# Kernel optimization log

Measured on AMD Instinct MI355X. Metric: run time of the kernel, lower is better.

The kernel has to match this reference:

```python
import jax, jax.numpy as jnp
import numpy as np

B, N_FEAT, SEQ, E, H, V = 32, 196, 64, 1024, 1024, 32000


def setup_inputs() -> dict:
    key = jax.random.key(0)
    ks = jax.random.split(key, 16)
    s = 0.02
    return {
        "features": jax.random.normal(ks[0], (B, N_FEAT, E), jnp.float32),
        "captions": jax.random.randint(ks[1], (B, SEQ), 0, V),
        "max_seq_length": SEQ,
        # decoder embedding table (vocab, embed)
        "emb": jax.random.normal(ks[2], (V, E), jnp.float32) * s,
        # attention MLP: Linear(E->H), Tanh, Linear(H->1)
        "Wa1": jax.random.normal(ks[3], (H, E), jnp.float32) * s,
        "ba1": jnp.zeros((H,), jnp.float32),
        "Wa2": jax.random.normal(ks[4], (1, H), jnp.float32) * s,
        "ba2": jnp.zeros((1,), jnp.float32),
        # GRU (1 layer), input = concat(word_emb, context) -> E + H
        "W_ih": jax.random.normal(ks[5], (3 * H, E + H), jnp.float32) * s,
        "W_hh": jax.random.normal(ks[6], (3 * H, H), jnp.float32) * s,
        "b_ih": jnp.zeros((3 * H,), jnp.float32),
        "b_hh": jnp.zeros((3 * H,), jnp.float32),
        # output projection Linear(H -> V)
        "W_fc": jax.random.normal(ks[7], (V, H), jnp.float32) * s,
        "b_fc": jnp.zeros((V,), jnp.float32),
    }


def reference(features, captions, max_seq_length, emb, Wa1, ba1, Wa2, ba2,
              W_ih, W_hh, b_ih, b_hh, W_fc, b_fc):
    # words: (B, S, E)
    words = emb[captions]
    # combined: (B, N_FEAT + S, E)
    combined = jnp.concatenate([features, words], axis=1)
    # attention scores over the combined tokens, softmax along token axis
    scores = jnp.tanh(combined @ Wa1.T + ba1) @ Wa2.T + ba2   # (B, M, 1)
    A = jax.nn.softmax(scores, axis=1)                         # (B, M, 1)
    # context h0 = A^T @ combined -> (B, E); used both as GRU h0 and per-step context
    h0 = jnp.sum(A * combined, axis=1)
    context = h0

    def gru_cell(x, h):
        gi = x @ W_ih.T + b_ih          # (B, 3H)
        gh = h @ W_hh.T + b_hh          # (B, 3H)
        ir, iz, inn = jnp.split(gi, 3, axis=-1)
        hr, hz, hn = jnp.split(gh, 3, axis=-1)
        r = jax.nn.sigmoid(ir + hr)
        z = jax.nn.sigmoid(iz + hz)
        n = jnp.tanh(inn + r * hn)
        return (1.0 - z) * n + z * h

    def step(carry, _):
        input_word, h = carry
        x = jnp.concatenate([emb[input_word], context], axis=-1)  # (B, E+H)
        h_new = gru_cell(x, h)
        out = h_new @ W_fc.T + b_fc                               # (B, V)
        # greedy feedback (eval path / no teacher forcing)
        next_word = jnp.argmax(out, axis=-1)
        return (next_word, h_new), out

    init = (captions[:, 0], h0)
    (_, _), outs = jax.lax.scan(step, init, None, length=max_seq_length - 1)
    outs = jnp.transpose(outs, (1, 0, 2))                         # (B, S-1, V)
    bsz = captions.shape[0]
    vocab = W_fc.shape[0]
    outputs = jnp.concatenate(
        [jnp.zeros((bsz, 1, vocab), outs.dtype), outs], axis=1)   # t=0 stays zero
    return outputs, A
```

## Files before the change

kernel.cpp:

```cpp
#include <hip/hip_runtime.h>
#include <hip/hip_bf16.h>

typedef unsigned long long ull;
typedef unsigned int uint;

#define NB 32
#define NFEAT 196
#define SEQL 64
#define ED 1024
#define HD 1024
#define VOC 32000
#define NCOMB 260
#define NROWS (NB*NCOMB)
#define NTILE 2000

typedef __attribute__((ext_vector_type(8))) short s16x8;
typedef __attribute__((ext_vector_type(4))) float f32x4;
typedef __attribute__((ext_vector_type(4))) uint  u32x4;

union FragU { u32x4 u; s16x8 s; };

#define DOT4(acc, wv, xv) acc = fmaf((wv).x,(xv).x, fmaf((wv).y,(xv).y, fmaf((wv).z,(xv).z, fmaf((wv).w,(xv).w,(acc)))))

__device__ __forceinline__ uint enc_f32(float f) {
    uint u = __float_as_uint(f);
    return (u & 0x80000000u) ? ~u : (u | 0x80000000u);
}
__device__ __forceinline__ ull shflxor64(ull v, int m) {
    uint lo = __shfl_xor((uint)v, m);
    uint hi = __shfl_xor((uint)(v >> 32), m);
    return (((ull)hi) << 32) | (ull)lo;
}

__device__ __forceinline__ void split2(float a, float b, uint& hi, uint& lo) {
    __hip_bfloat162 h2 = __float22bfloat162_rn(make_float2(a, b));
    float2 hf = __bfloat1622float2(h2);
    __hip_bfloat162 l2 = __float22bfloat162_rn(make_float2(a - hf.x, b - hf.y));
    hi = *(uint*)&h2;
    lo = *(uint*)&l2;
}

__global__ void __launch_bounds__(256) k_build(
    const float* __restrict__ features, const int* __restrict__ captions,
    const float* __restrict__ emb, float* __restrict__ combined,
    float* __restrict__ out)
{
    const int bid = blockIdx.x;
    const int t = threadIdx.x;
    if (bid < NROWS) {
        const int b = bid / NCOMB;
        const int i = bid - b*NCOMB;
        const float* src = (i < NFEAT)
            ? (features + ((size_t)(b*NFEAT + i))*ED)
            : (emb + (size_t)captions[b*SEQL + (i - NFEAT)]*ED);
        float4* dst4 = (float4*)(combined + (size_t)bid*ED);
        const float4* s4 = (const float4*)src;
        dst4[t] = s4[t];
    } else {
        const int z = bid - NROWS;
        const int m = z*1024 + t*4;
        if (m < NB*VOC) {
            const int b = m / VOC;
            const int v = m - b*VOC;
            float4 zz = make_float4(0.f,0.f,0.f,0.f);
            *(float4*)(out + (size_t)b*((size_t)SEQL*VOC) + v) = zz;
        }
    }
}

__global__ void __launch_bounds__(256) k_pack_w1(
    const float* __restrict__ Wa1, uint* __restrict__ W1hi, uint* __restrict__ W1lo)
{
    const int eid = blockIdx.x*256 + threadIdx.x;
    const int lane = eid & 63;
    const int ks = (eid >> 6) & 31;
    const int ct = eid >> 11;
    const int c = ct*16 + (lane & 15);
    const int k0 = ks*32 + ((lane >> 4) & 3)*4;
    const float4 wa = *(const float4*)&Wa1[(size_t)c*ED + k0];
    const float4 wb = *(const float4*)&Wa1[(size_t)c*ED + k0 + 16];
    uint hi[4], lo[4];
    split2(wa.x, wa.y, hi[0], lo[0]);
    split2(wa.z, wa.w, hi[1], lo[1]);
    split2(wb.x, wb.y, hi[2], lo[2]);
    split2(wb.z, wb.w, hi[3], lo[3]);
    *(u32x4*)&W1hi[(size_t)eid*4] = (u32x4){hi[0], hi[1], hi[2], hi[3]};
    *(u32x4*)&W1lo[(size_t)eid*4] = (u32x4){lo[0], lo[1], lo[2], lo[3]};
}

__global__ void __launch_bounds__(256) k_pack_wfc(
    const float* __restrict__ W_fc, uint* __restrict__ Whi, uint* __restrict__ Wlo)
{
    const int eid = blockIdx.x*256 + threadIdx.x;
    const int lane = eid & 63;
    const int ks = (eid >> 6) & 31;
    const int tile = eid >> 11;
    const int row = tile*16 + (lane & 15);
    const int k0 = ks*32 + ((lane >> 4) & 3)*4;
    const float4 wa = *(const float4*)&W_fc[(size_t)row*HD + k0];
    const float4 wb = *(const float4*)&W_fc[(size_t)row*HD + k0 + 16];
    uint hi[4], lo[4];
    split2(wa.x, wa.y, hi[0], lo[0]);
    split2(wa.z, wa.w, hi[1], lo[1]);
    split2(wb.x, wb.y, hi[2], lo[2]);
    split2(wb.z, wb.w, hi[3], lo[3]);
    *(u32x4*)&Whi[(size_t)eid*4] = (u32x4){hi[0], hi[1], hi[2], hi[3]};
    *(u32x4*)&Wlo[(size_t)eid*4] = (u32x4){lo[0], lo[1], lo[2], lo[3]};
}

__global__ void __launch_bounds__(256) k_attn_mfma(
    const float* __restrict__ combined, const uint* __restrict__ W1hi,
    const uint* __restrict__ W1lo, const float* __restrict__ ba1,
    const float* __restrict__ Wa2, float* __restrict__ partials)
{
    const int t = threadIdx.x;
    const int w = t >> 6, l = t & 63;
    const int lane16 = l & 15, qk = (l >> 4) & 3;
    const int rt = blockIdx.x*4 + w;
    const int cg = blockIdx.y;

    const float* Arow = combined + (size_t)(rt*16 + lane16)*ED;
    const u32x4* bh_base = (const u32x4*)W1hi + (size_t)(cg*4)*32*64 + l;
    const u32x4* bl_base = (const u32x4*)W1lo + (size_t)(cg*4)*32*64 + l;

    f32x4 acc[4];
#pragma unroll
    for (int i = 0; i < 4; ++i) acc[i] = (f32x4){0.f,0.f,0.f,0.f};

#pragma unroll 2
    for (int ks = 0; ks < 32; ++ks) {
        const int k0 = ks*32 + qk*4;
        const float4 aa = *(const float4*)(Arow + k0);
        const float4 ab = *(const float4*)(Arow + k0 + 16);
        FragU ahi, alo;
        uint h0,l0_,h1,l1_,h2,l2_,h3,l3_;
        split2(aa.x, aa.y, h0, l0_);
        split2(aa.z, aa.w, h1, l1_);
        split2(ab.x, ab.y, h2, l2_);
        split2(ab.z, ab.w, h3, l3_);
        ahi.u = (u32x4){h0, h1, h2, h3};
        alo.u = (u32x4){l0_, l1_, l2_, l3_};
#pragma unroll
        for (int i = 0; i < 4; ++i) {
            FragU bh_, bl_;
            bh_.u = bh_base[((size_t)i*32 + ks)*64];
            bl_.u = bl_base[((size_t)i*32 + ks)*64];
            acc[i] = __builtin_amdgcn_mfma_f32_16x16x32_bf16(ahi.s, bh_.s, acc[i], 0, 0, 0);
            acc[i] = __builtin_amdgcn_mfma_f32_16x16x32_bf16(ahi.s, bl_.s, acc[i], 0, 0, 0);
            acc[i] = __builtin_amdgcn_mfma_f32_16x16x32_bf16(alo.s, bh_.s, acc[i], 0, 0, 0);
        }
    }

    float s[4];
#pragma unroll
    for (int r = 0; r < 4; ++r) {
        float sum = 0.f;
#pragma unroll
        for (int i = 0; i < 4; ++i) {
            const int col = cg*64 + i*16 + lane16;
            sum += tanhf(acc[i][r] + ba1[col]) * Wa2[col];
        }
        s[r] = sum;
    }
#pragma unroll
    for (int m = 1; m <= 8; m <<= 1)
#pragma unroll
        for (int r = 0; r < 4; ++r) s[r] += __shfl_xor(s[r], m);
    if (lane16 == 0) {
#pragma unroll
        for (int r = 0; r < 4; ++r)
            partials[(size_t)(rt*16 + qk*4 + r)*16 + cg] = s[r];
    }
}

__global__ void __launch_bounds__(256) k_attn_finish(
    const float* __restrict__ partials, const float* __restrict__ combined,
    const int* __restrict__ captions,
    float* __restrict__ A_out, float* __restrict__ h0,
    float* __restrict__ ctx, ull* __restrict__ slots0)
{
    const int b = blockIdx.x, t = threadIdx.x;
    __shared__ float sc[NCOMB];
    __shared__ float red[256];

    for (int i = t; i < NCOMB; i += 256) {
        float s = 0.f;
        const float* pr = partials + (size_t)(b*NCOMB + i)*16;
#pragma unroll
        for (int g = 0; g < 16; ++g) s += pr[g];
        sc[i] = s;
    }
    __syncthreads();
    float m = -1e30f;
    for (int i = t; i < NCOMB; i += 256) m = fmaxf(m, sc[i]);
    red[t] = m; __syncthreads();
    for (int s2 = 128; s2 > 0; s2 >>= 1) {
        if (t < s2) red[t] = fmaxf(red[t], red[t+s2]);
        __syncthreads();
    }
    m = red[0]; __syncthreads();
    float ssum = 0.f;
    for (int i = t; i < NCOMB; i += 256) { float e = expf(sc[i] - m); sc[i] = e; ssum += e; }
    red[t] = ssum; __syncthreads();
    for (int s2 = 128; s2 > 0; s2 >>= 1) {
        if (t < s2) red[t] += red[t+s2];
        __syncthreads();
    }
    const float S = red[0]; __syncthreads();
    for (int i = t; i < NCOMB; i += 256) {
        const float a = sc[i] / S;
        sc[i] = a;
        A_out[b*NCOMB + i] = a;
    }
    __syncthreads();
    for (int e = t; e < HD; e += 256) {
        float acc = 0.f;
        const float* cb = combined + (size_t)b*NCOMB*ED + e;
        for (int i = 0; i < NCOMB; ++i) acc = fmaf(sc[i], cb[(size_t)i*ED], acc);
        h0[(size_t)b*HD + e] = acc;
        ctx[(size_t)b*HD + e] = acc;
    }
    if (t == 0) {
        slots0[0*NB + b] = (ull)(~(uint)captions[b*SEQL]);
#pragma unroll
        for (int g = 1; g < 8; ++g) slots0[g*NB + b] = 0ull;
    }
}

__global__ void __launch_bounds__(256) k_gru(
    const float* __restrict__ emb, const float* __restrict__ ctx,
    const float* __restrict__ W_ih, const float* __restrict__ W_hh,
    const float* __restrict__ b_ih, const float* __restrict__ b_hh,
    const float* __restrict__ h_prev, float* __restrict__ h_next,
    const ull* __restrict__ slots_prev, ull* __restrict__ slots_cur,
    uint* __restrict__ Hhi, uint* __restrict__ Hlo)
{
    __shared__ int word_s[NB];
    const int t = threadIdx.x;
    if (t < NB) {
        ull best = 0ull;
#pragma unroll
        for (int g = 0; g < 8; ++g) {
            ull k = slots_prev[g*NB + t];
            best = (k > best) ? k : best;
        }
        word_s[t] = (int)(~(uint)best);
    }
    if (blockIdx.x == 0) slots_cur[t] = 0ull;
    __syncthreads();

    const int j = blockIdx.x;
    const int w = t >> 6, l = t & 63;
    const int b0 = w*8;

    float a[4][8];
#pragma unroll
    for (int g = 0; g < 4; ++g)
#pragma unroll
        for (int i = 0; i < 8; ++i) a[g][i] = 0.f;

    const float* Wr = W_ih + (size_t)j*(ED+HD);
    const float* Wz = W_ih + (size_t)(HD + j)*(ED+HD);
    const float* Wn = W_ih + (size_t)(2*HD + j)*(ED+HD);
#pragma unroll
    for (int q = 0; q < 8; ++q) {
        const int k = q*256 + l*4;
        const float4 wr = *(const float4*)(Wr + k);
        const float4 wz = *(const float4*)(Wz + k);
        const float4 wn = *(const float4*)(Wn + k);
#pragma unroll
        for (int i = 0; i < 8; ++i) {
            const int b = b0 + i;
            const float* xs = (q < 4) ? (emb + (size_t)word_s[b]*ED + k)
                                      : (ctx + (size_t)b*HD + (k - ED));
            const float4 xv = *(const float4*)xs;
            DOT4(a[0][i], wr, xv);
            DOT4(a[1][i], wz, xv);
            DOT4(a[2][i], wn, xv);
        }
    }
    const float* Ur = W_hh + (size_t)j*HD;
    const float* Uz = W_hh + (size_t)(HD + j)*HD;
    const float* Un = W_hh + (size_t)(2*HD + j)*HD;
#pragma unroll
    for (int q = 0; q < 4; ++q) {
        const int k = q*256 + l*4;
        const float4 ur = *(const float4*)(Ur + k);
        const float4 uz = *(const float4*)(Uz + k);
        const float4 un = *(const float4*)(Un + k);
#pragma unroll
        for (int i = 0; i < 8; ++i) {
            const int b = b0 + i;
            const float4 hv = *(const float4*)(h_prev + (size_t)b*HD + k);
            DOT4(a[0][i], ur, hv);
            DOT4(a[1][i], uz, hv);
            DOT4(a[3][i], un, hv);
        }
    }
    int s = (l >> 5) & 1;
    int ib = s*4;
    float tA[4][4];
#pragma unroll
    for (int g = 0; g < 4; ++g)
#pragma unroll
        for (int ii = 0; ii < 4; ++ii) {
            const float send = a[g][(1^s)*4 + ii];
            tA[g][ii] = a[g][s*4 + ii] + __shfl_xor(send, 32);
        }
    s = (l >> 4) & 1; ib += s*2;
    float tB[4][2];
#pragma unroll
    for (int g = 0; g < 4; ++g)
#pragma unroll
        for (int jj = 0; jj < 2; ++jj) {
            const float send = tA[g][(1^s)*2 + jj];
            tB[g][jj] = tA[g][s*2 + jj] + __shfl_xor(send, 16);
        }
    s = (l >> 3) & 1; ib += s;
    float fg[4];
#pragma unroll
    for (int g = 0; g < 4; ++g) {
        const float send = tB[g][1^s];
        fg[g] = tB[g][s] + __shfl_xor(send, 8);
    }
#pragma unroll
    for (int mm = 4; mm >= 1; mm >>= 1)
#pragma unroll
        for (int g = 0; g < 4; ++g) fg[g] += __shfl_xor(fg[g], mm);

    if ((l & 7) == 0) {
        const int b = b0 + ib;
        const float rg = 1.f/(1.f + expf(-(fg[0] + b_ih[j]      + b_hh[j])));
        const float zg = 1.f/(1.f + expf(-(fg[1] + b_ih[HD+j]   + b_hh[HD+j])));
        const float ng = tanhf(fg[2] + b_ih[2*HD+j] + rg*(fg[3] + b_hh[2*HD+j]));
        const float hp = h_prev[(size_t)b*HD + j];
        const float hv = (1.f - zg)*ng + zg*hp;
        h_next[(size_t)b*HD + j] = hv;
        __hip_bfloat16 hb = __float2bfloat16(hv);
        const float hf = __bfloat162float(hb);
        __hip_bfloat16 lb = __float2bfloat16(hv - hf);
        const int bh = b >> 4;
        const int ks = j >> 5;
        const int qk2 = (j >> 2) & 3;
        const int elem = (j & 3) + 4*((j >> 4) & 1);
        const size_t ei = (((size_t)(bh*32 + ks))*64 + qk2*16 + (b & 15))*8 + elem;
        ((ushort*)Hhi)[ei] = *(const ushort*)&hb;
        ((ushort*)Hlo)[ei] = *(const ushort*)&lb;
    }
}

__global__ void __launch_bounds__(256) k_logits(
    const float* __restrict__ W_fc, const uint* __restrict__ Wfchi,
    const uint* __restrict__ Wfclo, const uint* __restrict__ Hhi,
    const uint* __restrict__ Hlo, const float* __restrict__ b_fc,
    float* __restrict__ out, ull* __restrict__ slots_cur, int tstep, int packed)
{
    __shared__ float sm[32][68];
    const int t = threadIdx.x;
    const int w = t >> 6, l = t & 63;
    const int lane16 = l & 15, qk = (l >> 4) & 3;
    const int tile = blockIdx.x*4 + w;
    const int row = tile*16 + lane16;

    const u32x4* hh0 = (const u32x4*)Hhi + l;
    const u32x4* hl0 = (const u32x4*)Hlo + l;
    const u32x4* hh1 = (const u32x4*)Hhi + 2048 + l;
    const u32x4* hl1 = (const u32x4*)Hlo + 2048 + l;

    f32x4 acc0 = {0.f,0.f,0.f,0.f};
    f32x4 acc1 = {0.f,0.f,0.f,0.f};

    if (packed) {
        const u32x4* WH = (const u32x4*)Wfchi + (size_t)tile*32*64 + l;
        const u32x4* WL = (const u32x4*)Wfclo + (size_t)tile*32*64 + l;
#pragma unroll 2
        for (int ks = 0; ks < 32; ++ks) {
            FragU whi, wlo, b0h, b0l, b1h, b1l;
            whi.u = WH[ks*64];
            wlo.u = WL[ks*64];
            b0h.u = hh0[ks*64];
            b0l.u = hl0[ks*64];
            b1h.u = hh1[ks*64];
            b1l.u = hl1[ks*64];
            acc0 = __builtin_amdgcn_mfma_f32_16x16x32_bf16(whi.s, b0h.s, acc0, 0, 0, 0);
            acc0 = __builtin_amdgcn_mfma_f32_16x16x32_bf16(whi.s, b0l.s, acc0, 0, 0, 0);
            acc0 = __builtin_amdgcn_mfma_f32_16x16x32_bf16(wlo.s, b0h.s, acc0, 0, 0, 0);
            acc1 = __builtin_amdgcn_mfma_f32_16x16x32_bf16(whi.s, b1h.s, acc1, 0, 0, 0);
            acc1 = __builtin_amdgcn_mfma_f32_16x16x32_bf16(whi.s, b1l.s, acc1, 0, 0, 0);
            acc1 = __builtin_amdgcn_mfma_f32_16x16x32_bf16(wlo.s, b1h.s, acc1, 0, 0, 0);
        }
    } else {
        const float* Wrow = W_fc + (size_t)row*HD;
#pragma unroll 2
        for (int ks = 0; ks < 32; ++ks) {
            const int k0 = ks*32 + qk*4;
            const float4 wa = *(const float4*)(Wrow + k0);
            const float4 wb = *(const float4*)(Wrow + k0 + 16);
            FragU whi, wlo;
            uint h0,l0_,h1,l1_,h2,l2_,h3,l3_;
            split2(wa.x, wa.y, h0, l0_);
            split2(wa.z, wa.w, h1, l1_);
            split2(wb.x, wb.y, h2, l2_);
            split2(wb.z, wb.w, h3, l3_);
            whi.u = (u32x4){h0, h1, h2, h3};
            wlo.u = (u32x4){l0_, l1_, l2_, l3_};
            FragU b0h, b0l, b1h, b1l;
            b0h.u = hh0[ks*64];
            b0l.u = hl0[ks*64];
            b1h.u = hh1[ks*64];
            b1l.u = hl1[ks*64];
            acc0 = __builtin_amdgcn_mfma_f32_16x16x32_bf16(whi.s, b0h.s, acc0, 0, 0, 0);
            acc0 = __builtin_amdgcn_mfma_f32_16x16x32_bf16(whi.s, b0l.s, acc0, 0, 0, 0);
            acc0 = __builtin_amdgcn_mfma_f32_16x16x32_bf16(wlo.s, b0h.s, acc0, 0, 0, 0);
            acc1 = __builtin_amdgcn_mfma_f32_16x16x32_bf16(whi.s, b1h.s, acc1, 0, 0, 0);
            acc1 = __builtin_amdgcn_mfma_f32_16x16x32_bf16(whi.s, b1l.s, acc1, 0, 0, 0);
            acc1 = __builtin_amdgcn_mfma_f32_16x16x32_bf16(wlo.s, b1h.s, acc1, 0, 0, 0);
        }
    }

    {
        const int rbase = w*16 + qk*4;
        const float4 bias = *(const float4*)&b_fc[blockIdx.x*64 + rbase];
        *(float4*)&sm[lane16][rbase] = make_float4(
            acc0[0] + bias.x, acc0[1] + bias.y, acc0[2] + bias.z, acc0[3] + bias.w);
        *(float4*)&sm[16 + lane16][rbase] = make_float4(
            acc1[0] + bias.x, acc1[1] + bias.y, acc1[2] + bias.z, acc1[3] + bias.w);
    }
    __syncthreads();
    {
        const int b = t >> 3;
        const int rl0 = (t & 7)*8;
        const int vbase = blockIdx.x*64 + rl0;
        float v[8];
        ull bk = 0ull;
#pragma unroll
        for (int e = 0; e < 8; ++e) {
            v[e] = sm[b][rl0 + e];
            const ull key = (((ull)enc_f32(v[e])) << 32) | (ull)(~(uint)(vbase + e));
            bk = (key > bk) ? key : bk;
        }
        float* dst = out + (size_t)b*((size_t)SEQL*VOC) + (size_t)tstep*VOC + vbase;
        ((float4*)dst)[0] = make_float4(v[0], v[1], v[2], v[3]);
        ((float4*)dst)[1] = make_float4(v[4], v[5], v[6], v[7]);
#pragma unroll
        for (int mm = 4; mm >= 1; mm >>= 1) {
            const ull o = shflxor64(bk, mm);
            bk = (o > bk) ? o : bk;
        }
        if ((t & 7) == 0) atomicMax(slots_cur + (blockIdx.x & 7)*NB + b, bk);
    }
}

extern "C" void kernel_launch(void* const* d_in, const int* in_sizes, int n_in,
                              void* d_out, int out_size, void* d_ws, size_t ws_size,
                              hipStream_t stream)
{
    const float* features = (const float*)d_in[0];
    const int*   captions = (const int*)d_in[1];
    const float* emb  = (const float*)d_in[3];
    const float* Wa1  = (const float*)d_in[4];
    const float* ba1  = (const float*)d_in[5];
    const float* Wa2  = (const float*)d_in[6];
    const float* W_ih = (const float*)d_in[8];
    const float* W_hh = (const float*)d_in[9];
    const float* b_ih = (const float*)d_in[10];
    const float* b_hh = (const float*)d_in[11];
    const float* W_fc = (const float*)d_in[12];
    const float* b_fc = (const float*)d_in[13];

    float* out = (float*)d_out;
    float* A_out = out + (size_t)NB*SEQL*VOC;

    char* wsp = (char*)d_ws;
    float* combined = (float*)wsp;  wsp += (size_t)NROWS*ED*4;
    float* partials = (float*)wsp;  wsp += (size_t)NROWS*16*4;
    float* hbuf0    = (float*)wsp;  wsp += (size_t)NB*HD*4;
    float* hbuf1    = (float*)wsp;  wsp += (size_t)NB*HD*4;
    float* ctx      = (float*)wsp;  wsp += (size_t)NB*HD*4;
    ull*   slots    = (ull*)wsp;    wsp += 2*8*NB*sizeof(ull);
    uint*  Hhi      = (uint*)wsp;   wsp += (size_t)4096*16;
    uint*  Hlo      = (uint*)wsp;   wsp += (size_t)4096*16;
    uint*  W1hi     = (uint*)wsp;   wsp += (size_t)131072*16;
    uint*  W1lo     = (uint*)wsp;   wsp += (size_t)131072*16;
    uint*  Wfchi    = (uint*)wsp;   wsp += (size_t)NTILE*32*64*16;
    uint*  Wfclo    = (uint*)wsp;   wsp += (size_t)NTILE*32*64*16;
    size_t packed_need = (size_t)(wsp - (char*)d_ws);
    const int packed = (ws_size >= packed_need) ? 1 : 0;

    k_build<<<NROWS + 1000, 256, 0, stream>>>(features, captions, emb, combined, out);
    k_pack_w1<<<512, 256, 0, stream>>>(Wa1, W1hi, W1lo);
    if (packed)
        k_pack_wfc<<<NTILE*32*64/256, 256, 0, stream>>>(W_fc, Wfchi, Wfclo);
    k_attn_mfma<<<dim3(130, 16), 256, 0, stream>>>(combined, W1hi, W1lo, ba1, Wa2, partials);
    k_attn_finish<<<NB, 256, 0, stream>>>(partials, combined, captions,
                                          A_out, hbuf0, ctx, slots);
    for (int t = 1; t < SEQL; ++t) {
        const float* hp = (t & 1) ? hbuf0 : hbuf1;
        float*       hn = (t & 1) ? hbuf1 : hbuf0;
        const ull* sp = slots + (size_t)((t - 1) & 1)*8*NB;
        ull*       scur = slots + (size_t)(t & 1)*8*NB;
        k_gru<<<1024, 256, 0, stream>>>(emb, ctx, W_ih, W_hh, b_ih, b_hh,
                                        hp, hn, sp, scur, Hhi, Hlo);
        k_logits<<<500, 256, 0, stream>>>(W_fc, Wfchi, Wfclo, Hhi, Hlo, b_fc,
                                          out, scur, t, packed);
    }
}
```

Before: 4.442 ms.

## Split logits K across waves and widen attention column groups per block

The logits kernel now gives each block two 16-row vocab tiles, each split over two K halves handled by separate waves. The halves are merged through shared memory before bias add and argmax, and the grid doubles to 1000 blocks. The aim is more parallelism and shorter per-wave dependent MFMA chains in the latency-bound per-step logits GEMM, at the cost of an extra barrier and an LDS reduction. Separately, the attention MFMA kernel has each block compute two column groups so the A-fragment split is reused, halving its grid.

```diff
diff --git a/kernel.cpp b/kernel.cpp
--- a/kernel.cpp
+++ b/kernel.cpp
@@ -117,15 +117,17 @@
     const int w = t >> 6, l = t & 63;
     const int lane16 = l & 15, qk = (l >> 4) & 3;
     const int rt = blockIdx.x*4 + w;
-    const int cg = blockIdx.y;
+    const int cg0 = blockIdx.y*2;
 
     const float* Arow = combined + (size_t)(rt*16 + lane16)*ED;
-    const u32x4* bh_base = (const u32x4*)W1hi + (size_t)(cg*4)*32*64 + l;
-    const u32x4* bl_base = (const u32x4*)W1lo + (size_t)(cg*4)*32*64 + l;
-
-    f32x4 acc[4];
-#pragma unroll
-    for (int i = 0; i < 4; ++i) acc[i] = (f32x4){0.f,0.f,0.f,0.f};
+    const u32x4* bh_base = (const u32x4*)W1hi + l;
+    const u32x4* bl_base = (const u32x4*)W1lo + l;
+
+    f32x4 acc[2][4];
+#pragma unroll
+    for (int c = 0; c < 2; ++c)
+#pragma unroll
+        for (int i = 0; i < 4; ++i) acc[c][i] = (f32x4){0.f,0.f,0.f,0.f};
 
 #pragma unroll 2
     for (int ks = 0; ks < 32; ++ks) {
@@ -141,35 +143,43 @@
         ahi.u = (u32x4){h0, h1, h2, h3};
         alo.u = (u32x4){l0_, l1_, l2_, l3_};
 #pragma unroll
-        for (int i = 0; i < 4; ++i) {
-            FragU bh_, bl_;
-            bh_.u = bh_base[((size_t)i*32 + ks)*64];
-            bl_.u = bl_base[((size_t)i*32 + ks)*64];
-            acc[i] = __builtin_amdgcn_mfma_f32_16x16x32_bf16(ahi.s, bh_.s, acc[i], 0, 0, 0);
-            acc[i] = __builtin_amdgcn_mfma_f32_16x16x32_bf16(ahi.s, bl_.s, acc[i], 0, 0, 0);
-            acc[i] = __builtin_amdgcn_mfma_f32_16x16x32_bf16(alo.s, bh_.s, acc[i], 0, 0, 0);
-        }
-    }
-
-    float s[4];
-#pragma unroll
-    for (int r = 0; r < 4; ++r) {
-        float sum = 0.f;
-#pragma unroll
-        for (int i = 0; i < 4; ++i) {
-            const int col = cg*64 + i*16 + lane16;
-            sum += tanhf(acc[i][r] + ba1[col]) * Wa2[col];
-        }
-        s[r] = sum;
-    }
-#pragma unroll
-    for (int m = 1; m <= 8; m <<= 1)
-#pragma unroll
-        for (int r = 0; r < 4; ++r) s[r] += __shfl_xor(s[r], m);
-    if (lane16 == 0) {
-#pragma unroll
-        for (int r = 0; r < 4; ++r)
-            partials[(size_t)(rt*16 + qk*4 + r)*16 + cg] = s[r];
+        for (int c = 0; c < 2; ++c) {
+#pragma unroll
+            for (int i = 0; i < 4; ++i) {
+                const size_t idx = (((size_t)((cg0 + c)*4 + i))*32 + ks)*64;
+                FragU bh_, bl_;
+                bh_.u = bh_base[idx];
+                bl_.u = bl_base[idx];
+                acc[c][i] = __builtin_amdgcn_mfma_f32_16x16x32_bf16(ahi.s, bh_.s, acc[c][i], 0, 0, 0);
+                acc[c][i] = __builtin_amdgcn_mfma_f32_16x16x32_bf16(ahi.s, bl_.s, acc[c][i], 0, 0, 0);
+                acc[c][i] = __builtin_amdgcn_mfma_f32_16x16x32_bf16(alo.s, bh_.s, acc[c][i], 0, 0, 0);
+            }
+        }
+    }
+
+#pragma unroll
+    for (int c = 0; c < 2; ++c) {
+        const int cg = cg0 + c;
+        float s[4];
+#pragma unroll
+        for (int r = 0; r < 4; ++r) {
+            float sum = 0.f;
+#pragma unroll
+            for (int i = 0; i < 4; ++i) {
+                const int col = cg*64 + i*16 + lane16;
+                sum += tanhf(acc[c][i][r] + ba1[col]) * Wa2[col];
+            }
+            s[r] = sum;
+        }
+#pragma unroll
+        for (int m = 1; m <= 8; m <<= 1)
+#pragma unroll
+            for (int r = 0; r < 4; ++r) s[r] += __shfl_xor(s[r], m);
+        if (lane16 == 0) {
+#pragma unroll
+            for (int r = 0; r < 4; ++r)
+                partials[(size_t)(rt*16 + qk*4 + r)*16 + cg] = s[r];
+        }
     }
 }
 
@@ -355,26 +365,29 @@
     const uint* __restrict__ Hlo, const float* __restrict__ b_fc,
     float* __restrict__ out, ull* __restrict__ slots_cur, int tstep, int packed)
 {
-    __shared__ float sm[32][68];
+    __shared__ float sm[32][33];
+    __shared__ float mergebuf[2][64][8];
     const int t = threadIdx.x;
     const int w = t >> 6, l = t & 63;
     const int lane16 = l & 15, qk = (l >> 4) & 3;
-    const int tile = blockIdx.x*4 + w;
+    const int tt = w & 1;
+    const int kh = w >> 1;
+    const int tile = blockIdx.x*2 + tt;
     const int row = tile*16 + lane16;
 
-    const u32x4* hh0 = (const u32x4*)Hhi + l;
-    const u32x4* hl0 = (const u32x4*)Hlo + l;
-    const u32x4* hh1 = (const u32x4*)Hhi + 2048 + l;
-    const u32x4* hl1 = (const u32x4*)Hlo + 2048 + l;
+    const u32x4* hh0 = (const u32x4*)Hhi + (size_t)(kh*16)*64 + l;
+    const u32x4* hl0 = (const u32x4*)Hlo + (size_t)(kh*16)*64 + l;
+    const u32x4* hh1 = (const u32x4*)Hhi + (size_t)(32 + kh*16)*64 + l;
+    const u32x4* hl1 = (const u32x4*)Hlo + (size_t)(32 + kh*16)*64 + l;
 
     f32x4 acc0 = {0.f,0.f,0.f,0.f};
     f32x4 acc1 = {0.f,0.f,0.f,0.f};
 
     if (packed) {
-        const u32x4* WH = (const u32x4*)Wfchi + (size_t)tile*32*64 + l;
-        const u32x4* WL = (const u32x4*)Wfclo + (size_t)tile*32*64 + l;
+        const u32x4* WH = (const u32x4*)Wfchi + ((size_t)tile*32 + kh*16)*64 + l;
+        const u32x4* WL = (const u32x4*)Wfclo + ((size_t)tile*32 + kh*16)*64 + l;
 #pragma unroll 2
-        for (int ks = 0; ks < 32; ++ks) {
+        for (int ks = 0; ks < 16; ++ks) {
             FragU whi, wlo, b0h, b0l, b1h, b1l;
             whi.u = WH[ks*64];
             wlo.u = WL[ks*64];
@@ -392,8 +405,8 @@
     } else {
         const float* Wrow = W_fc + (size_t)row*HD;
 #pragma unroll 2
-        for (int ks = 0; ks < 32; ++ks) {
-            const int k0 = ks*32 + qk*4;
+        for (int ks = 0; ks < 16; ++ks) {
+            const int k0 = (kh*16 + ks)*32 + qk*4;
             const float4 wa = *(const float4*)(Wrow + k0);
             const float4 wb = *(const float4*)(Wrow + k0 + 16);
             FragU whi, wlo;
@@ -418,36 +431,44 @@
         }
     }
 
-    {
-        const int rbase = w*16 + qk*4;
-        const float4 bias = *(const float4*)&b_fc[blockIdx.x*64 + rbase];
-        *(float4*)&sm[lane16][rbase] = make_float4(
-            acc0[0] + bias.x, acc0[1] + bias.y, acc0[2] + bias.z, acc0[3] + bias.w);
-        *(float4*)&sm[16 + lane16][rbase] = make_float4(
-            acc1[0] + bias.x, acc1[1] + bias.y, acc1[2] + bias.z, acc1[3] + bias.w);
+    if (kh == 1) {
+        float* rr = &mergebuf[tt][l][0];
+        *(float4*)&rr[0] = make_float4(acc0[0], acc0[1], acc0[2], acc0[3]);
+        *(float4*)&rr[4] = make_float4(acc1[0], acc1[1], acc1[2], acc1[3]);
+    }
+    __syncthreads();
+    if (kh == 0) {
+        const float* rr = &mergebuf[tt][l][0];
+        const float4 bias = *(const float4*)&b_fc[tile*16 + qk*4];
+#pragma unroll
+        for (int r = 0; r < 4; ++r) {
+            const int rloc = tt*16 + qk*4 + r;
+            const float bb = (&bias.x)[r];
+            sm[lane16][rloc]      = acc0[r] + rr[r]     + bb;
+            sm[16 + lane16][rloc] = acc1[r] + rr[4 + r] + bb;
+        }
     }
     __syncthreads();
     {
         const int b = t >> 3;
-        const int rl0 = (t & 7)*8;
-        const int vbase = blockIdx.x*64 + rl0;
-        float v[8];
+        const int rq = t & 7;
+        const int vbase = blockIdx.x*32 + rq*4;
+        float v[4];
         ull bk = 0ull;
 #pragma unroll
-        for (int e = 0; e < 8; ++e) {
-            v[e] = sm[b][rl0 + e];
+        for (int e = 0; e < 4; ++e) {
+            v[e] = sm[b][rq*4 + e];
             const ull key = (((ull)enc_f32(v[e])) << 32) | (ull)(~(uint)(vbase + e));
             bk = (key > bk) ? key : bk;
         }
-        float* dst = out + (size_t)b*((size_t)SEQL*VOC) + (size_t)tstep*VOC + vbase;
-        ((float4*)dst)[0] = make_float4(v[0], v[1], v[2], v[3]);
-        ((float4*)dst)[1] = make_float4(v[4], v[5], v[6], v[7]);
+        *(float4*)&out[(size_t)b*((size_t)SEQL*VOC) + (size_t)tstep*VOC + vbase] =
+            make_float4(v[0], v[1], v[2], v[3]);
 #pragma unroll
         for (int mm = 4; mm >= 1; mm >>= 1) {
             const ull o = shflxor64(bk, mm);
             bk = (o > bk) ? o : bk;
         }
-        if ((t & 7) == 0) atomicMax(slots_cur + (blockIdx.x & 7)*NB + b, bk);
+        if (rq == 0) atomicMax(slots_cur + (blockIdx.x & 7)*NB + b, bk);
     }
 }
 
@@ -491,7 +512,7 @@
     k_pack_w1<<<512, 256, 0, stream>>>(Wa1, W1hi, W1lo);
     if (packed)
         k_pack_wfc<<<NTILE*32*64/256, 256, 0, stream>>>(W_fc, Wfchi, Wfclo);
-    k_attn_mfma<<<dim3(130, 16), 256, 0, stream>>>(combined, W1hi, W1lo, ba1, Wa2, partials);
+    k_attn_mfma<<<dim3(130, 8), 256, 0, stream>>>(combined, W1hi, W1lo, ba1, Wa2, partials);
     k_attn_finish<<<NB, 256, 0, stream>>>(partials, combined, captions,
                                           A_out, hbuf0, ctx, slots);
     for (int t = 1; t < SEQL; ++t) {
@@ -501,7 +522,7 @@
         ull*       scur = slots + (size_t)(t & 1)*8*NB;
         k_gru<<<1024, 256, 0, stream>>>(emb, ctx, W_ih, W_hh, b_ih, b_hh,
                                         hp, hn, sp, scur, Hhi, Hlo);
-        k_logits<<<500, 256, 0, stream>>>(W_fc, Wfchi, Wfclo, Hhi, Hlo, b_fc,
-                                          out, scur, t, packed);
-    }
-}
+        k_logits<<<NTILE/2, 256, 0, stream>>>(W_fc, Wfchi, Wfclo, Hhi, Hlo, b_fc,
+                                              out, scur, t, packed);
+    }
+}
```

Result: slower. 4.565 ms (+2.8%).

## Fuse logits and next-step GRU via grid barrier; precompute context input gates

Applied to the files above, without the earlier changes.

Merges the per-step logits and the following GRU update into one kernel. Blocks write logits and argmax partials, then meet at an atomic-counter grid barrier, after which each block computes the GRU for a slice of hidden units for the next step. The constant context part of the input-gate product (W_ih times ctx plus b_ih) is now computed once up front in a new kernel instead of at every step. The attention MFMA kernel also handles two column groups per block. This halves the number of per-step launches and drops the redundant context GEMV, but the spin barrier assumes all 500 blocks are resident at the same time, and the GRU work is spread over only 500 blocks.

```diff
diff --git a/kernel.cpp b/kernel.cpp
--- a/kernel.cpp
+++ b/kernel.cpp
@@ -13,6 +13,7 @@
 #define NCOMB 260
 #define NROWS (NB*NCOMB)
 #define NTILE 2000
+#define STEPBLK 500
 
 typedef __attribute__((ext_vector_type(8))) short s16x8;
 typedef __attribute__((ext_vector_type(4))) float f32x4;
@@ -43,7 +44,7 @@
 __global__ void __launch_bounds__(256) k_build(
     const float* __restrict__ features, const int* __restrict__ captions,
     const float* __restrict__ emb, float* __restrict__ combined,
-    float* __restrict__ out)
+    float* __restrict__ out, uint* __restrict__ counters)
 {
     const int bid = blockIdx.x;
     const int t = threadIdx.x;
@@ -56,7 +57,7 @@
         float4* dst4 = (float4*)(combined + (size_t)bid*ED);
         const float4* s4 = (const float4*)src;
         dst4[t] = s4[t];
-    } else {
+    } else if (bid < NROWS + 1000) {
         const int z = bid - NROWS;
         const int m = z*1024 + t*4;
         if (m < NB*VOC) {
@@ -65,6 +66,8 @@
             float4 zz = make_float4(0.f,0.f,0.f,0.f);
             *(float4*)(out + (size_t)b*((size_t)SEQL*VOC) + v) = zz;
         }
+    } else {
+        if (t < SEQL) counters[t] = 0u;
     }
 }
 
@@ -117,15 +120,17 @@
     const int w = t >> 6, l = t & 63;
     const int lane16 = l & 15, qk = (l >> 4) & 3;
     const int rt = blockIdx.x*4 + w;
-    const int cg = blockIdx.y;
+    const int cg0 = blockIdx.y*2;
 
     const float* Arow = combined + (size_t)(rt*16 + lane16)*ED;
-    const u32x4* bh_base = (const u32x4*)W1hi + (size_t)(cg*4)*32*64 + l;
-    const u32x4* bl_base = (const u32x4*)W1lo + (size_t)(cg*4)*32*64 + l;
-
-    f32x4 acc[4];
-#pragma unroll
-    for (int i = 0; i < 4; ++i) acc[i] = (f32x4){0.f,0.f,0.f,0.f};
+    const u32x4* bh_base = (const u32x4*)W1hi + l;
+    const u32x4* bl_base = (const u32x4*)W1lo + l;
+
+    f32x4 acc[2][4];
+#pragma unroll
+    for (int c = 0; c < 2; ++c)
+#pragma unroll
+        for (int i = 0; i < 4; ++i) acc[c][i] = (f32x4){0.f,0.f,0.f,0.f};
 
 #pragma unroll 2
     for (int ks = 0; ks < 32; ++ks) {
@@ -141,35 +146,43 @@
         ahi.u = (u32x4){h0, h1, h2, h3};
         alo.u = (u32x4){l0_, l1_, l2_, l3_};
 #pragma unroll
-        for (int i = 0; i < 4; ++i) {
-            FragU bh_, bl_;
-            bh_.u = bh_base[((size_t)i*32 + ks)*64];
-            bl_.u = bl_base[((size_t)i*32 + ks)*64];
-            acc[i] = __builtin_amdgcn_mfma_f32_16x16x32_bf16(ahi.s, bh_.s, acc[i], 0, 0, 0);
-            acc[i] = __builtin_amdgcn_mfma_f32_16x16x32_bf16(ahi.s, bl_.s, acc[i], 0, 0, 0);
-            acc[i] = __builtin_amdgcn_mfma_f32_16x16x32_bf16(alo.s, bh_.s, acc[i], 0, 0, 0);
-        }
-    }
-
-    float s[4];
-#pragma unroll
-    for (int r = 0; r < 4; ++r) {
-        float sum = 0.f;
-#pragma unroll
-        for (int i = 0; i < 4; ++i) {
-            const int col = cg*64 + i*16 + lane16;
-            sum += tanhf(acc[i][r] + ba1[col]) * Wa2[col];
-        }
-        s[r] = sum;
-    }
-#pragma unroll
-    for (int m = 1; m <= 8; m <<= 1)
-#pragma unroll
-        for (int r = 0; r < 4; ++r) s[r] += __shfl_xor(s[r], m);
-    if (lane16 == 0) {
-#pragma unroll
-        for (int r = 0; r < 4; ++r)
-            partials[(size_t)(rt*16 + qk*4 + r)*16 + cg] = s[r];
+        for (int c = 0; c < 2; ++c) {
+#pragma unroll
+            for (int i = 0; i < 4; ++i) {
+                const size_t idx = (((size_t)((cg0 + c)*4 + i))*32 + ks)*64;
+                FragU bh_, bl_;
+                bh_.u = bh_base[idx];
+                bl_.u = bl_base[idx];
+                acc[c][i] = __builtin_amdgcn_mfma_f32_16x16x32_bf16(ahi.s, bh_.s, acc[c][i], 0, 0, 0);
+                acc[c][i] = __builtin_amdgcn_mfma_f32_16x16x32_bf16(ahi.s, bl_.s, acc[c][i], 0, 0, 0);
+                acc[c][i] = __builtin_amdgcn_mfma_f32_16x16x32_bf16(alo.s, bh_.s, acc[c][i], 0, 0, 0);
+            }
+        }
+    }
+
+#pragma unroll
+    for (int c = 0; c < 2; ++c) {
+        const int cg = cg0 + c;
+        float s[4];
+#pragma unroll
+        for (int r = 0; r < 4; ++r) {
+            float sum = 0.f;
+#pragma unroll
+            for (int i = 0; i < 4; ++i) {
+                const int col = cg*64 + i*16 + lane16;
+                sum += tanhf(acc[c][i][r] + ba1[col]) * Wa2[col];
+            }
+            s[r] = sum;
+        }
+#pragma unroll
+        for (int m = 1; m <= 8; m <<= 1)
+#pragma unroll
+            for (int r = 0; r < 4; ++r) s[r] += __shfl_xor(s[r], m);
+        if (lane16 == 0) {
+#pragma unroll
+            for (int r = 0; r < 4; ++r)
+                partials[(size_t)(rt*16 + qk*4 + r)*16 + cg] = s[r];
+        }
     }
 }
 
@@ -225,6 +238,56 @@
 #pragma unroll
         for (int g = 1; g < 8; ++g) slots0[g*NB + b] = 0ull;
     }
+}
+
+__global__ void __launch_bounds__(256) k_gictx(
+    const float* __restrict__ W_ih, const float* __restrict__ b_ih,
+    const float* __restrict__ ctx, float* __restrict__ gictx)
+{
+    const int jj = blockIdx.x;
+    const int t = threadIdx.x;
+    const int w = t >> 6, l = t & 63;
+    const int b0 = w*8;
+    const float* Wrow = W_ih + (size_t)jj*(ED+HD) + ED;
+
+    float a[8];
+#pragma unroll
+    for (int i = 0; i < 8; ++i) a[i] = 0.f;
+#pragma unroll
+    for (int q = 0; q < 4; ++q) {
+        const int k = q*256 + l*4;
+        const float4 wv = *(const float4*)(Wrow + k);
+#pragma unroll
+        for (int i = 0; i < 8; ++i) {
+            const float4 xv = *(const float4*)(ctx + (size_t)(b0 + i)*HD + k);
+            DOT4(a[i], wv, xv);
+        }
+    }
+    int s = (l >> 5) & 1;
+    int ib = s*4;
+    float tA[4];
+#pragma unroll
+    for (int ii = 0; ii < 4; ++ii) {
+        const float send = a[(1^s)*4 + ii];
+        tA[ii] = a[s*4 + ii] + __shfl_xor(send, 32);
+    }
+    s = (l >> 4) & 1; ib += s*2;
+    float tB[2];
+#pragma unroll
+    for (int jj2 = 0; jj2 < 2; ++jj2) {
+        const float send = tA[(1^s)*2 + jj2];
+        tB[jj2] = tA[s*2 + jj2] + __shfl_xor(send, 16);
+    }
+    s = (l >> 3) & 1; ib += s;
+    float fg;
+    {
+        const float send = tB[1^s];
+        fg = tB[s] + __shfl_xor(send, 8);
+    }
+#pragma unroll
+    for (int mm = 4; mm >= 1; mm >>= 1) fg += __shfl_xor(fg, mm);
+    if ((l & 7) == 0)
+        gictx[(size_t)jj*NB + (b0 + ib)] = fg + b_ih[jj];
 }
 
 __global__ void __launch_bounds__(256) k_gru(
@@ -349,106 +412,255 @@
     }
 }
 
-__global__ void __launch_bounds__(256) k_logits(
-    const float* __restrict__ W_fc, const uint* __restrict__ Wfchi,
-    const uint* __restrict__ Wfclo, const uint* __restrict__ Hhi,
-    const uint* __restrict__ Hlo, const float* __restrict__ b_fc,
-    float* __restrict__ out, ull* __restrict__ slots_cur, int tstep, int packed)
+__device__ __forceinline__ void gru_one_j(
+    int j, const int* word_s, const float* __restrict__ emb,
+    const float* __restrict__ W_ih, const float* __restrict__ W_hh,
+    const float* __restrict__ gictx, const float* __restrict__ b_hh,
+    const float* __restrict__ hp, float* __restrict__ hn,
+    uint* __restrict__ Hhi, uint* __restrict__ Hlo, int w, int l)
+{
+    const int b0 = w*8;
+    float a[4][8];
+#pragma unroll
+    for (int g = 0; g < 4; ++g)
+#pragma unroll
+        for (int i = 0; i < 8; ++i) a[g][i] = 0.f;
+
+    const float* Wr = W_ih + (size_t)j*(ED+HD);
+    const float* Wz = W_ih + (size_t)(HD + j)*(ED+HD);
+    const float* Wn = W_ih + (size_t)(2*HD + j)*(ED+HD);
+#pragma unroll
+    for (int q = 0; q < 4; ++q) {
+        const int k = q*256 + l*4;
+        const float4 wr = *(const float4*)(Wr + k);
+        const float4 wz = *(const float4*)(Wz + k);
+        const float4 wn = *(const float4*)(Wn + k);
+#pragma unroll
+        for (int i = 0; i < 8; ++i) {
+            const float4 xv = *(const float4*)(emb + (size_t)word_s[b0+i]*ED + k);
+            DOT4(a[0][i], wr, xv);
+            DOT4(a[1][i], wz, xv);
+            DOT4(a[2][i], wn, xv);
+        }
+    }
+    const float* Ur = W_hh + (size_t)j*HD;
+    const float* Uz = W_hh + (size_t)(HD + j)*HD;
+    const float* Un = W_hh + (size_t)(2*HD + j)*HD;
+#pragma unroll
+    for (int q = 0; q < 4; ++q) {
+        const int k = q*256 + l*4;
+        const float4 ur = *(const float4*)(Ur + k);
+        const float4 uz = *(const float4*)(Uz + k);
+        const float4 un = *(const float4*)(Un + k);
+#pragma unroll
+        for (int i = 0; i < 8; ++i) {
+            const float4 hv = *(const float4*)(hp + (size_t)(b0+i)*HD + k);
+            DOT4(a[0][i], ur, hv);
+            DOT4(a[1][i], uz, hv);
+            DOT4(a[3][i], un, hv);
+        }
+    }
+    int s = (l >> 5) & 1;
+    int ib = s*4;
+    float tA[4][4];
+#pragma unroll
+    for (int g = 0; g < 4; ++g)
+#pragma unroll
+        for (int ii = 0; ii < 4; ++ii) {
+            const float send = a[g][(1^s)*4 + ii];
+            tA[g][ii] = a[g][s*4 + ii] + __shfl_xor(send, 32);
+        }
+    s = (l >> 4) & 1; ib += s*2;
+    float tB[4][2];
+#pragma unroll
+    for (int g = 0; g < 4; ++g)
+#pragma unroll
+        for (int jj = 0; jj < 2; ++jj) {
+            const float send = tA[g][(1^s)*2 + jj];
+            tB[g][jj] = tA[g][s*2 + jj] + __shfl_xor(send, 16);
+        }
+    s = (l >> 3) & 1; ib += s;
+    float fg[4];
+#pragma unroll
+    for (int g = 0; g < 4; ++g) {
+        const float send = tB[g][1^s];
+        fg[g] = tB[g][s] + __shfl_xor(send, 8);
+    }
+#pragma unroll
+    for (int mm = 4; mm >= 1; mm >>= 1)
+#pragma unroll
+        for (int g = 0; g < 4; ++g) fg[g] += __shfl_xor(fg[g], mm);
+
+    if ((l & 7) == 0) {
+        const int b = b0 + ib;
+        const float gcr = gictx[(size_t)j*NB + b];
+        const float gcz = gictx[(size_t)(HD + j)*NB + b];
+        const float gcn = gictx[(size_t)(2*HD + j)*NB + b];
+        const float rg = 1.f/(1.f + expf(-(fg[0] + gcr + b_hh[j])));
+        const float zg = 1.f/(1.f + expf(-(fg[1] + gcz + b_hh[HD+j])));
+        const float ng = tanhf(fg[2] + gcn + rg*(fg[3] + b_hh[2*HD+j]));
+        const float hpv = hp[(size_t)b*HD + j];
+        const float hv = (1.f - zg)*ng + zg*hpv;
+        hn[(size_t)b*HD + j] = hv;
+        __hip_bfloat16 hb = __float2bfloat16(hv);
+        const float hf = __bfloat162float(hb);
+        __hip_bfloat16 lb = __float2bfloat16(hv - hf);
+        const int bh = b >> 4;
+        const int ks = j >> 5;
+        const int qk2 = (j >> 2) & 3;
+        const int elem = (j & 3) + 4*((j >> 4) & 1);
+        const size_t ei = (((size_t)(bh*32 + ks))*64 + qk2*16 + (b & 15))*8 + elem;
+        ((ushort*)Hhi)[ei] = *(const ushort*)&hb;
+        ((ushort*)Hlo)[ei] = *(const ushort*)&lb;
+    }
+}
+
+__global__ void __launch_bounds__(256, 2) k_step(
+    const uint* __restrict__ Wfchi, const uint* __restrict__ Wfclo,
+    const float* __restrict__ W_fc,
+    uint* __restrict__ Hhi, uint* __restrict__ Hlo,
+    const float* __restrict__ b_fc, float* __restrict__ out,
+    ull* __restrict__ slots, uint* __restrict__ counters,
+    const float* __restrict__ emb, const float* __restrict__ W_ih,
+    const float* __restrict__ W_hh, const float* __restrict__ gictx,
+    const float* __restrict__ b_hh,
+    const float* __restrict__ hp, float* __restrict__ hn,
+    int tstep, int packed)
 {
     __shared__ float sm[32][68];
     const int t = threadIdx.x;
     const int w = t >> 6, l = t & 63;
     const int lane16 = l & 15, qk = (l >> 4) & 3;
     const int tile = blockIdx.x*4 + w;
-    const int row = tile*16 + lane16;
-
-    const u32x4* hh0 = (const u32x4*)Hhi + l;
-    const u32x4* hl0 = (const u32x4*)Hlo + l;
-    const u32x4* hh1 = (const u32x4*)Hhi + 2048 + l;
-    const u32x4* hl1 = (const u32x4*)Hlo + 2048 + l;
-
-    f32x4 acc0 = {0.f,0.f,0.f,0.f};
-    f32x4 acc1 = {0.f,0.f,0.f,0.f};
-
-    if (packed) {
-        const u32x4* WH = (const u32x4*)Wfchi + (size_t)tile*32*64 + l;
-        const u32x4* WL = (const u32x4*)Wfclo + (size_t)tile*32*64 + l;
+    ull* scur = slots + (size_t)(tstep & 1)*8*NB;
+
+    {
+        const u32x4* hh0 = (const u32x4*)Hhi + l;
+        const u32x4* hl0 = (const u32x4*)Hlo + l;
+        const u32x4* hh1 = (const u32x4*)Hhi + 2048 + l;
+        const u32x4* hl1 = (const u32x4*)Hlo + 2048 + l;
+
+        f32x4 acc0 = {0.f,0.f,0.f,0.f};
+        f32x4 acc1 = {0.f,0.f,0.f,0.f};
+
+        if (packed) {
+            const u32x4* WH = (const u32x4*)Wfchi + (size_t)tile*32*64 + l;
+            const u32x4* WL = (const u32x4*)Wfclo + (size_t)tile*32*64 + l;
 #pragma unroll 2
-        for (int ks = 0; ks < 32; ++ks) {
-            FragU whi, wlo, b0h, b0l, b1h, b1l;
-            whi.u = WH[ks*64];
-            wlo.u = WL[ks*64];
-            b0h.u = hh0[ks*64];
-            b0l.u = hl0[ks*64];
-            b1h.u = hh1[ks*64];
-            b1l.u = hl1[ks*64];
-            acc0 = __builtin_amdgcn_mfma_f32_16x16x32_bf16(whi.s, b0h.s, acc0, 0, 0, 0);
-            acc0 = __builtin_amdgcn_mfma_f32_16x16x32_bf16(whi.s, b0l.s, acc0, 0, 0, 0);
-            acc0 = __builtin_amdgcn_mfma_f32_16x16x32_bf16(wlo.s, b0h.s, acc0, 0, 0, 0);
-            acc1 = __builtin_amdgcn_mfma_f32_16x16x32_bf16(whi.s, b1h.s, acc1, 0, 0, 0);
-            acc1 = __builtin_amdgcn_mfma_f32_16x16x32_bf16(whi.s, b1l.s, acc1, 0, 0, 0);
-            acc1 = __builtin_amdgcn_mfma_f32_16x16x32_bf16(wlo.s, b1h.s, acc1, 0, 0, 0);
-        }
-    } else {
-        const float* Wrow = W_fc + (size_t)row*HD;
+            for (int ks = 0; ks < 32; ++ks) {
+                FragU whi, wlo, b0h, b0l, b1h, b1l;
+                whi.u = WH[ks*64];
+                wlo.u = WL[ks*64];
+                b0h.u = hh0[ks*64];
+                b0l.u = hl0[ks*64];
+                b1h.u = hh1[ks*64];
+                b1l.u = hl1[ks*64];
+                acc0 = __builtin_amdgcn_mfma_f32_16x16x32_bf16(whi.s, b0h.s, acc0, 0, 0, 0);
+                acc0 = __builtin_amdgcn_mfma_f32_16x16x32_bf16(whi.s, b0l.s, acc0, 0, 0, 0);
+                acc0 = __builtin_amdgcn_mfma_f32_16x16x32_bf16(wlo.s, b0h.s, acc0, 0, 0, 0);
+                acc1 = __builtin_amdgcn_mfma_f32_16x16x32_bf16(whi.s, b1h.s, acc1, 0, 0, 0);
+                acc1 = __builtin_amdgcn_mfma_f32_16x16x32_bf16(whi.s, b1l.s, acc1, 0, 0, 0);
+                acc1 = __builtin_amdgcn_mfma_f32_16x16x32_bf16(wlo.s, b1h.s, acc1, 0, 0, 0);
+            }
+        } else {
+            const float* Wrow = W_fc + (size_t)(tile*16 + lane16)*HD;
 #pragma unroll 2
-        for (int ks = 0; ks < 32; ++ks) {
-            const int k0 = ks*32 + qk*4;
-            const float4 wa = *(const float4*)(Wrow + k0);
-            const float4 wb = *(const float4*)(Wrow + k0 + 16);
-            FragU whi, wlo;
-            uint h0,l0_,h1,l1_,h2,l2_,h3,l3_;
-            split2(wa.x, wa.y, h0, l0_);
-            split2(wa.z, wa.w, h1, l1_);
-            split2(wb.x, wb.y, h2, l2_);
-            split2(wb.z, wb.w, h3, l3_);
-            whi.u = (u32x4){h0, h1, h2, h3};
-            wlo.u = (u32x4){l0_, l1_, l2_, l3_};
-            FragU b0h, b0l, b1h, b1l;
-            b0h.u = hh0[ks*64];
-            b0l.u = hl0[ks*64];
-            b1h.u = hh1[ks*64];
-            b1l.u = hl1[ks*64];
-            acc0 = __builtin_amdgcn_mfma_f32_16x16x32_bf16(whi.s, b0h.s, acc0, 0, 0, 0);
-            acc0 = __builtin_amdgcn_mfma_f32_16x16x32_bf16(whi.s, b0l.s, acc0, 0, 0, 0);
-            acc0 = __builtin_amdgcn_mfma_f32_16x16x32_bf16(wlo.s, b0h.s, acc0, 0, 0, 0);
-            acc1 = __builtin_amdgcn_mfma_f32_16x16x32_bf16(whi.s, b1h.s, acc1, 0, 0, 0);
-            acc1 = __builtin_amdgcn_mfma_f32_16x16x32_bf16(whi.s, b1l.s, acc1, 0, 0, 0);
-            acc1 = __builtin_amdgcn_mfma_f32_16x16x32_bf16(wlo.s, b1h.s, acc1, 0, 0, 0);
-        }
-    }
-
-    {
-        const int rbase = w*16 + qk*4;
-        const float4 bias = *(const float4*)&b_fc[blockIdx.x*64 + rbase];
-        *(float4*)&sm[lane16][rbase] = make_float4(
-            acc0[0] + bias.x, acc0[1] + bias.y, acc0[2] + bias.z, acc0[3] + bias.w);
-        *(float4*)&sm[16 + lane16][rbase] = make_float4(
-            acc1[0] + bias.x, acc1[1] + bias.y, acc1[2] + bias.z, acc1[3] + bias.w);
-    }
+            for (int ks = 0; ks < 32; ++ks) {
+                const int k0 = ks*32 + qk*4;
+                const float4 wa = *(const float4*)(Wrow + k0);
+                const float4 wb = *(const float4*)(Wrow + k0 + 16);
+                FragU whi, wlo;
+                uint h0,l0_,h1,l1_,h2,l2_,h3,l3_;
+                split2(wa.x, wa.y, h0, l0_);
+                split2(wa.z, wa.w, h1, l1_);
+                split2(wb.x, wb.y, h2, l2_);
+                split2(wb.z, wb.w, h3, l3_);
+                whi.u = (u32x4){h0, h1, h2, h3};
+                wlo.u = (u32x4){l0_, l1_, l2_, l3_};
+                FragU b0h, b0l, b1h, b1l;
+                b0h.u = hh0[ks*64];
+                b0l.u = hl0[ks*64];
+                b1h.u = hh1[ks*64];
+                b1l.u = hl1[ks*64];
+                acc0 = __builtin_amdgcn_mfma_f32_16x16x32_bf16(whi.s, b0h.s, acc0, 0, 0, 0);
+                acc0 = __builtin_amdgcn_mfma_f32_16x16x32_bf16(whi.s, b0l.s, acc0, 0, 0, 0);
+                acc0 = __builtin_amdgcn_mfma_f32_16x16x32_bf16(wlo.s, b0h.s, acc0, 0, 0, 0);
+                acc1 = __builtin_amdgcn_mfma_f32_16x16x32_bf16(whi.s, b1h.s, acc1, 0, 0, 0);
+                acc1 = __builtin_amdgcn_mfma_f32_16x16x32_bf16(whi.s, b1l.s, acc1, 0, 0, 0);
+                acc1 = __builtin_amdgcn_mfma_f32_16x16x32_bf16(wlo.s, b1h.s, acc1, 0, 0, 0);
+            }
+        }
+
+        {
+            const int rbase = w*16 + qk*4;
+            const float4 bias = *(const float4*)&b_fc[blockIdx.x*64 + rbase];
+            *(float4*)&sm[lane16][rbase] = make_float4(
+                acc0[0] + bias.x, acc0[1] + bias.y, acc0[2] + bias.z, acc0[3] + bias.w);
+            *(float4*)&sm[16 + lane16][rbase] = make_float4(
+                acc1[0] + bias.x, acc1[1] + bias.y, acc1[2] + bias.z, acc1[3] + bias.w);
+        }
+        __syncthreads();
+        {
+            const int b = t >> 3;
+            const int rl0 = (t & 7)*8;
+            const int vbase = blockIdx.x*64 + rl0;
+            float v[8];
+            ull bk = 0ull;
+#pragma unroll
+            for (int e = 0; e < 8; ++e) {
+                v[e] = sm[b][rl0 + e];
+                const ull key = (((ull)enc_f32(v[e])) << 32) | (ull)(~(uint)(vbase + e));
+                bk = (key > bk) ? key : bk;
+            }
+            float* dst = out + (size_t)b*((size_t)SEQL*VOC) + (size_t)tstep*VOC + vbase;
+            ((float4*)dst)[0] = make_float4(v[0], v[1], v[2], v[3]);
+            ((float4*)dst)[1] = make_float4(v[4], v[5], v[6], v[7]);
+#pragma unroll
+            for (int mm = 4; mm >= 1; mm >>= 1) {
+                const ull o = shflxor64(bk, mm);
+                bk = (o > bk) ? o : bk;
+            }
+            if ((t & 7) == 0) atomicMax(scur + (blockIdx.x & 7)*NB + b, bk);
+        }
+    }
+
+    if (tstep == SEQL - 1) return;
+
+    __threadfence();
     __syncthreads();
-    {
-        const int b = t >> 3;
-        const int rl0 = (t & 7)*8;
-        const int vbase = blockIdx.x*64 + rl0;
-        float v[8];
-        ull bk = 0ull;
-#pragma unroll
-        for (int e = 0; e < 8; ++e) {
-            v[e] = sm[b][rl0 + e];
-            const ull key = (((ull)enc_f32(v[e])) << 32) | (ull)(~(uint)(vbase + e));
-            bk = (key > bk) ? key : bk;
-        }
-        float* dst = out + (size_t)b*((size_t)SEQL*VOC) + (size_t)tstep*VOC + vbase;
-        ((float4*)dst)[0] = make_float4(v[0], v[1], v[2], v[3]);
-        ((float4*)dst)[1] = make_float4(v[4], v[5], v[6], v[7]);
-#pragma unroll
-        for (int mm = 4; mm >= 1; mm >>= 1) {
-            const ull o = shflxor64(bk, mm);
-            bk = (o > bk) ? o : bk;
-        }
-        if ((t & 7) == 0) atomicMax(slots_cur + (blockIdx.x & 7)*NB + b, bk);
-    }
+    __shared__ uint rank_s;
+    if (t == 0) {
+        uint r = __hip_atomic_fetch_add(&counters[tstep], 1u,
+                                        __ATOMIC_ACQ_REL, __HIP_MEMORY_SCOPE_AGENT);
+        rank_s = r;
+        while (__hip_atomic_load(&counters[tstep], __ATOMIC_ACQUIRE,
+                                 __HIP_MEMORY_SCOPE_AGENT) < (uint)STEPBLK)
+            __builtin_amdgcn_s_sleep(8);
+    }
+    __syncthreads();
+    const int rank = (int)rank_s;
+
+    __shared__ int word_s[NB];
+    if (t < NB) {
+        ull best = 0ull;
+#pragma unroll
+        for (int g = 0; g < 8; ++g) {
+            ull k = __hip_atomic_load(&scur[g*NB + t], __ATOMIC_RELAXED,
+                                      __HIP_MEMORY_SCOPE_AGENT);
+            best = (k > best) ? k : best;
+        }
+        word_s[t] = (int)(~(uint)best);
+    }
+    if (rank == 0) {
+        ull* snext = slots + (size_t)((tstep + 1) & 1)*8*NB;
+        snext[t] = 0ull;
+    }
+    __syncthreads();
+
+    gru_one_j(rank,        word_s, emb, W_ih, W_hh, gictx, b_hh, hp, hn, Hhi, Hlo, w, l);
+    gru_one_j(500 + rank,  word_s, emb, W_ih, W_hh, gictx, b_hh, hp, hn, Hhi, Hlo, w, l);
+    if (rank < 24)
+        gru_one_j(1000 + rank, word_s, emb, W_ih, W_hh, gictx, b_hh, hp, hn, Hhi, Hlo, w, l);
 }
 
 extern "C" void kernel_launch(void* const* d_in, const int* in_sizes, int n_in,
@@ -482,26 +694,30 @@
     uint*  Hlo      = (uint*)wsp;   wsp += (size_t)4096*16;
     uint*  W1hi     = (uint*)wsp;   wsp += (size_t)131072*16;
     uint*  W1lo     = (uint*)wsp;   wsp += (size_t)131072*16;
+    float* gictx    = (float*)wsp;  wsp += (size_t)3*HD*NB*4;
+    uint*  counters = (uint*)wsp;   wsp += 64*sizeof(uint);
     uint*  Wfchi    = (uint*)wsp;   wsp += (size_t)NTILE*32*64*16;
     uint*  Wfclo    = (uint*)wsp;   wsp += (size_t)NTILE*32*64*16;
     size_t packed_need = (size_t)(wsp - (char*)d_ws);
     const int packed = (ws_size >= packed_need) ? 1 : 0;
 
-    k_build<<<NROWS + 1000, 256, 0, stream>>>(features, captions, emb, combined, out);
+    k_build<<<NROWS + 1001, 256, 0, stream>>>(features, captions, emb, combined,
+                                              out, counters);
     k_pack_w1<<<512, 256, 0, stream>>>(Wa1, W1hi, W1lo);
     if (packed)
         k_pack_wfc<<<NTILE*32*64/256, 256, 0, stream>>>(W_fc, Wfchi, Wfclo);
-    k_attn_mfma<<<dim3(130, 16), 256, 0, stream>>>(combined, W1hi, W1lo, ba1, Wa2, partials);
+    k_attn_mfma<<<dim3(130, 8), 256, 0, stream>>>(combined, W1hi, W1lo, ba1, Wa2, partials);
     k_attn_finish<<<NB, 256, 0, stream>>>(partials, combined, captions,
                                           A_out, hbuf0, ctx, slots);
+    k_gictx<<<3*HD, 256, 0, stream>>>(W_ih, b_ih, ctx, gictx);
+    k_gru<<<1024, 256, 0, stream>>>(emb, ctx, W_ih, W_hh, b_ih, b_hh,
+                                    hbuf0, hbuf1, slots, slots + 8*NB, Hhi, Hlo);
     for (int t = 1; t < SEQL; ++t) {
-        const float* hp = (t & 1) ? hbuf0 : hbuf1;
-        float*       hn = (t & 1) ? hbuf1 : hbuf0;
-        const ull* sp = slots + (size_t)((t - 1) & 1)*8*NB;
-        ull*       scur = slots + (size_t)(t & 1)*8*NB;
-        k_gru<<<1024, 256, 0, stream>>>(emb, ctx, W_ih, W_hh, b_ih, b_hh,
-                                        hp, hn, sp, scur, Hhi, Hlo);
-        k_logits<<<500, 256, 0, stream>>>(W_fc, Wfchi, Wfclo, Hhi, Hlo, b_fc,
-                                          out, scur, t, packed);
-    }
-}
+        const float* hp = (t & 1) ? hbuf1 : hbuf0;
+        float*       hn = (t & 1) ? hbuf0 : hbuf1;
+        k_step<<<STEPBLK, 256, 0, stream>>>(Wfchi, Wfclo, W_fc, Hhi, Hlo, b_fc,
+                                            out, slots, counters,
+                                            emb, W_ih, W_hh, gictx, b_hh,
+                                            hp, hn, t, packed);
+    }
+}
```

Measured after the change: 13.70 ms. 3.08x slower.
